# Performance work log

Measured on AMD Instinct MI355X. Metric: run time of the kernel, lower is better.

Reference implementation:

```python
import jax, jax.numpy as jnp
import numpy as np
import math

B, S, HID = 1, 4096, 2048
NH, NKV, HD = 16, 4, 128
SKETCH, TOPK = 640, 2048
EPS = 1e-6


def _dct_orthonormal(rows, cols, rng, sink=4, fsink=8):
    i = np.arange(rows)[:, None]
    j = np.arange(cols)[None, :]
    dct = np.cos(np.pi / cols * (j + 0.5) * i)
    dct[0, :] *= math.sqrt(1.0 / cols)
    dct[1:, :] *= math.sqrt(2.0 / cols)
    signs = rng.integers(0, 2, (1, cols)).astype(np.float64) * 2.0 - 1.0
    m = dct * signs
    m[:, :sink] *= 2.0
    m[:fsink, :] *= 1.5
    return m.astype(np.float32)


def setup_inputs() -> dict:
    key = jax.random.key(0)
    ks = jax.random.split(key, 8)
    rng = np.random.default_rng(0)
    # RoPE tables (b, s, 1, head_dim)
    pos = np.arange(S, dtype=np.float32)
    inv = 1.0 / (10000.0 ** (np.arange(0, HD, 2, dtype=np.float32) / HD))
    ang = pos[:, None] * inv[None, :]              # (S, HD/2)
    emb = np.concatenate([ang, ang], axis=-1)       # (S, HD)
    cos = np.broadcast_to(np.cos(emb)[None, :, None, :], (B, S, 1, HD)).copy()
    sin = np.broadcast_to(np.sin(emb)[None, :, None, :], (B, S, 1, HD)).copy()
    w = 0.02
    return {
        'hidden_states': jax.random.normal(ks[0], (B, S, HID), jnp.float32),
        'wq': jax.random.normal(ks[1], (HID, NH * HD), jnp.float32) * w,
        'wk': jax.random.normal(ks[2], (HID, NKV * HD), jnp.float32) * w,
        'wv': jax.random.normal(ks[3], (HID, NKV * HD), jnp.float32) * w,
        'wo': jax.random.normal(ks[4], (NH * HD, HID), jnp.float32) * w,
        'qn_w': jnp.ones((HD,), jnp.float32),
        'kn_w': jnp.ones((HD,), jnp.float32),
        's_w1': jax.random.normal(ks[5], (HID, 64), jnp.float32) * w,
        's_b1': jnp.zeros((64,), jnp.float32),
        's_w2': jax.random.normal(ks[6], (64, 1), jnp.float32) * w,
        's_b2': jnp.zeros((1,), jnp.float32),
        'sketch_scale': jnp.full((1,), 0.1, jnp.float32),
        'kron_a': jnp.asarray(_dct_orthonormal(20, 128, rng)),
        'kron_b': jnp.asarray(_dct_orthonormal(32, 256, rng)),
        'cos': jnp.asarray(cos),
        'sin': jnp.asarray(sin),
    }


def _rms_norm(x, w):
    var = jnp.mean(jnp.square(x), axis=-1, keepdims=True)
    return x * jax.lax.rsqrt(var + EPS) * w


def _rope(x, cos, sin):
    # x: (b, s, h, d); cos/sin: (b, s, 1, d)
    d2 = x.shape[-1] // 2
    rot = jnp.concatenate([-x[..., d2:], x[..., :d2]], axis=-1)
    return x * cos + rot * sin


def reference(hidden_states, wq, wk, wv, wo, qn_w, kn_w, s_w1, s_b1, s_w2, s_b2,
              sketch_scale, kron_a, kron_b, cos, sin):
    b, s, _ = hidden_states.shape
    # importance scorer with compression pressure bias
    logits = jnp.tanh(hidden_states @ s_w1 + s_b1) @ s_w2 + s_b2   # (b, s, 1)
    if s > SKETCH:
        logits = logits - math.log(s / SKETCH)
    iw = jax.nn.sigmoid(logits)                                    # (b, s, 1)

    q = (hidden_states @ wq).reshape(b, s, NH, HD)
    k = (hidden_states @ wk).reshape(b, s, NKV, HD)
    v = (hidden_states @ wv).reshape(b, s, NKV, HD)
    q = _rms_norm(q, qn_w)
    k = _rms_norm(k, kn_w)

    tk = min(s, TOPK)
    _, idx = jax.lax.top_k(logits[..., 0], tk)                     # (b, tk)
    ix = idx[:, :, None, None]
    k_detail = jnp.take_along_axis(k, ix, axis=1)                  # (b, tk, nkv, d)
    v_detail = jnp.take_along_axis(v, ix, axis=1)
    cos_det = jnp.take_along_axis(cos, ix, axis=1)                 # (b, tk, 1, d)
    sin_det = jnp.take_along_axis(sin, ix, axis=1)

    # Kronecker sketch of importance-weighted K/V over all tokens
    P = jnp.kron(kron_a, kron_b)[:, :s]                            # (640, s)
    kw = k * iw[..., None]
    vw = v * iw[..., None]
    k_sketch = jnp.einsum('bshd,ms->bmhd', kw, P) * sketch_scale
    v_sketch = jnp.einsum('bshd,ms->bmhd', vw, P) * sketch_scale

    q_rope = _rope(q, cos, sin)
    k_detail = _rope(k_detail, cos_det, sin_det)

    k_final = jnp.concatenate([k_detail, k_sketch], axis=1)        # (b, tk+640, nkv, d)
    v_final = jnp.concatenate([v_detail, v_sketch], axis=1)
    rep = NH // NKV
    k_final = jnp.repeat(k_final, rep, axis=2)                     # (b, L, nh, d)
    v_final = jnp.repeat(v_final, rep, axis=2)

    scores = jnp.einsum('bqhd,bkhd->bhqk', q_rope, k_final) / math.sqrt(HD)
    attn = jax.nn.softmax(scores, axis=-1)
    out = jnp.einsum('bhqk,bkhd->bqhd', attn, v_final).reshape(b, s, NH * HD)
    return out @ wo
```

## Files before the change

### kernel.cpp

```cpp
#include <hip/hip_runtime.h>
#include <math.h>

typedef _Float16 f16;
typedef f16 f16x8 __attribute__((ext_vector_type(8)));
typedef float f32x4 __attribute__((ext_vector_type(4)));

#define MFMA16(a,b,c) __builtin_amdgcn_mfma_f32_16x16x32_f16(a,b,c,0,0,0)

static __device__ __forceinline__ f16x8 ld8(const f16* p) { return *(const f16x8*)p; }

static __device__ __forceinline__ float exp2a(float x) {
    float r; asm("v_exp_f32 %0, %1" : "=v"(r) : "v"(x)); return r;
}

static __device__ __forceinline__ int xcd_remap(int flat, int nwg) {
    int q = nwg >> 3, r = nwg & 7;
    int xcd = flat & 7, pos = flat >> 3;
    return (xcd < r ? xcd * (q + 1) : r * (q + 1) + (xcd - r) * q) + pos;
}

#if __has_builtin(__builtin_amdgcn_global_load_lds)
#define GLL16(g, lptr) __builtin_amdgcn_global_load_lds((const __attribute__((address_space(1))) void*)(g), (__attribute__((address_space(3))) void*)(lptr), 16, 0, 0)
#else
#define GLL16(g, lptr) do { *(int4*)(lptr) = *(const int4*)(g); } while (0)
#endif

__global__ __launch_bounds__(256) void k_mlp1t(const float* __restrict__ h, const float* __restrict__ w1,
                                               const float* __restrict__ wq, const float* __restrict__ wk,
                                               const float* __restrict__ wv, const float* __restrict__ wo,
                                               double* __restrict__ part, f16* __restrict__ h16,
                                               f16* __restrict__ wqkvt, f16* __restrict__ wot) {
    int blk = blockIdx.x;
    int tid = threadIdx.x;
    if (blk < 512) {
        __shared__ float hs[64 * 68];
        __shared__ float ws[64 * 64];
        int rb = blk & 63, ks = blk >> 6;
        int jq = tid & 15, rt = tid >> 4;
        double acc[4][4];
        #pragma unroll
        for (int r = 0; r < 4; ++r)
            #pragma unroll
            for (int q = 0; q < 4; ++q) acc[r][q] = 0.0;

        float4 hreg[4], wreg[4];
        int hrow[4], hcq[4], wc[4], wq4[4];
        #pragma unroll
        for (int i = 0; i < 4; ++i) {
            int fl = i * 256 + tid;
            hrow[i] = fl >> 4; hcq[i] = fl & 15;
            wc[i] = fl >> 4;   wq4[i] = fl & 15;
        }
        #define LOADCH(c8) do {                                                                  \
            _Pragma("unroll")                                                                     \
            for (int i = 0; i < 4; ++i) {                                                         \
                hreg[i] = *(const float4*)&h[(size_t)(rb*64 + hrow[i])*2048 + ks*256 + (c8)*64 + hcq[i]*4]; \
                wreg[i] = *(const float4*)&w1[(size_t)(ks*256 + (c8)*64 + wc[i])*64 + wq4[i]*4];  \
            }                                                                                     \
        } while (0)

        LOADCH(0);
        for (int c8 = 0; c8 < 4; ++c8) {
            __syncthreads();
            #pragma unroll
            for (int i = 0; i < 4; ++i) {
                *(float4*)&hs[hrow[i]*68 + hcq[i]*4] = hreg[i];
                *(float4*)&ws[wc[i]*64 + wq4[i]*4] = wreg[i];
                const float* hp = (const float*)&hreg[i];
                f16 h4[4];
                #pragma unroll
                for (int z = 0; z < 4; ++z) h4[z] = (f16)hp[z];
                *(float*)&h16[(size_t)(rb*64 + hrow[i])*2048 + ks*256 + c8*64 + hcq[i]*4] = *(float*)h4;
                *(float*)(&h16[(size_t)(rb*64 + hrow[i])*2048 + ks*256 + c8*64 + hcq[i]*4 + 2]) = *(((float*)h4)+1);
            }
            __syncthreads();
            if (c8 < 3) LOADCH(c8 + 1);
            #pragma unroll 4
            for (int cg = 0; cg < 64; cg += 4) {
                float4 ha[4], wa[4];
                #pragma unroll
                for (int r = 0; r < 4; ++r) ha[r] = *(const float4*)&hs[(rt + 16*r)*68 + cg];
                #pragma unroll
                for (int cc = 0; cc < 4; ++cc) wa[cc] = *(const float4*)&ws[(cg + cc)*64 + jq*4];
                #pragma unroll
                for (int cc = 0; cc < 4; ++cc) {
                    const float* wap = (const float*)&wa[cc];
                    double wd0 = (double)wap[0], wd1 = (double)wap[1], wd2 = (double)wap[2], wd3 = (double)wap[3];
                    #pragma unroll
                    for (int r = 0; r < 4; ++r) {
                        double hv = (double)((const float*)&ha[r])[cc];
                        acc[r][0] = fma(hv, wd0, acc[r][0]);
                        acc[r][1] = fma(hv, wd1, acc[r][1]);
                        acc[r][2] = fma(hv, wd2, acc[r][2]);
                        acc[r][3] = fma(hv, wd3, acc[r][3]);
                    }
                }
            }
        }
        #pragma unroll
        for (int r = 0; r < 4; ++r)
            #pragma unroll
            for (int q = 0; q < 4; ++q)
                part[((size_t)ks*4096 + rb*64 + rt + 16*r)*64 + jq*4 + q] = acc[r][q];
        #undef LOADCH
    } else {
        __shared__ float tile[32][33];
        int tb = blk - 512;
        int bx = tb % 160;
        int y0 = (tb / 160) * 32;
        int tx = tid & 31, ty = tid >> 5;
        const float* in; int inCols, colBase, rowOff; f16* out;
        if (bx < 64)      { in = wq; inCols = 2048; colBase = bx * 32;        rowOff = colBase;        out = wqkvt; }
        else if (bx < 80) { in = wk; inCols = 512;  colBase = (bx - 64) * 32; rowOff = 2048 + colBase; out = wqkvt; }
        else if (bx < 96) { in = wv; inCols = 512;  colBase = (bx - 80) * 32; rowOff = 2560 + colBase; out = wqkvt; }
        else              { in = wo; inCols = 2048; colBase = (bx - 96) * 32; rowOff = colBase;        out = wot; }
        int x = colBase + tx;
        #pragma unroll
        for (int i = 0; i < 4; ++i)
            tile[ty + i*8][tx] = in[(size_t)(y0 + ty + i*8) * inCols + x];
        __syncthreads();
        #pragma unroll
        for (int i = 0; i < 4; ++i)
            out[(size_t)(rowOff + ty + i*8) * 2048 + y0 + tx] = (f16)tile[tx][ty + i*8];
    }
}

__global__ __launch_bounds__(256) void k_mlp2(const double* __restrict__ part, const float* __restrict__ b1,
                                              const float* __restrict__ w2, const float* __restrict__ b2,
                                              double* __restrict__ logitsD, float* __restrict__ iw) {
    int tid = threadIdx.x;
    int j = tid & 63, rq = tid >> 6;
    int row = blockIdx.x * 4 + rq;
    double s = 0.0;
    #pragma unroll
    for (int ks = 0; ks < 8; ++ks) s += part[((size_t)ks*4096 + row)*64 + j];
    double t = tanh(s + (double)b1[j]);
    double v = t * (double)w2[j];
    #pragma unroll
    for (int o = 32; o > 0; o >>= 1) v += __shfl_down(v, o);
    if (j == 0) {
        double lg = v + (double)b2[0] - 1.8562979903656263;
        logitsD[row] = lg;
        iw[row] = (float)(1.0 / (1.0 + exp(-lg)));
    }
}

__global__ __launch_bounds__(1024) void k_topk(const double* __restrict__ logitsD, int* __restrict__ sel) {
    __shared__ unsigned long long keys[4096];
    __shared__ unsigned int hist[2048];
    __shared__ unsigned int bcast[2];
    __shared__ unsigned int cA, cB;
    int tid = threadIdx.x;
    for (int i = tid; i < 4096; i += 1024) {
        unsigned long long u = (unsigned long long)__double_as_longlong(logitsD[i]);
        keys[i] = (u >> 63) ? ~u : (u | 0x8000000000000000ull);
    }
    if (tid == 0) { cA = 0; cB = 0; }
    unsigned long long Tpart = 0;
    unsigned int need = 2048;
    #pragma unroll 1
    for (int lvl = 0; lvl < 6; ++lvl) {
        int shift = (lvl < 5) ? (53 - 11*lvl) : 0;
        int width = (lvl < 5) ? 11 : 9;
        unsigned int nb = 1u << width;
        int hiShift = shift + width;
        for (int i = tid; i < (int)nb; i += 1024) hist[i] = 0;
        __syncthreads();
        for (int i = tid; i < 4096; i += 1024) {
            unsigned long long k = keys[i];
            bool cand = (lvl == 0) || ((k >> hiShift) == (Tpart >> hiShift));
            if (cand) atomicAdd(&hist[(unsigned int)(k >> shift) & (nb - 1u)], 1u);
        }
        __syncthreads();
        if (tid < 64) {
            int chunk = (int)nb >> 6;
            int base = (int)nb - (tid + 1) * chunk;
            unsigned int sum = 0;
            for (int jj = 0; jj < chunk; ++jj) sum += hist[base + jj];
            unsigned int pre = sum;
            #pragma unroll
            for (int o = 1; o < 64; o <<= 1) {
                unsigned int t = __shfl_up(pre, o);
                if (tid >= o) pre += t;
            }
            unsigned int preEx = pre - sum;
            if (preEx < need && need <= pre) {
                unsigned int cum = preEx;
                for (int jj = chunk - 1; jj >= 0; --jj) {
                    unsigned int c = hist[base + jj];
                    if (cum + c >= need) { bcast[0] = (unsigned int)(base + jj); bcast[1] = need - cum; break; }
                    cum += c;
                }
            }
        }
        __syncthreads();
        Tpart |= ((unsigned long long)bcast[0]) << shift;
        need = bcast[1];
        __syncthreads();
    }
    unsigned int G = 2048 - need;
    for (int i = tid; i < 4096; i += 1024) {
        unsigned long long k = keys[i];
        if (k > Tpart) { unsigned int p = atomicAdd(&cA, 1u); sel[p] = i; }
        else if (k == Tpart) { unsigned int q = atomicAdd(&cB, 1u); if (q < need) sel[G + q] = i; }
    }
}

__global__ __launch_bounds__(256) void k_gemm(const f16* __restrict__ A, const f16* __restrict__ Bt,
                                              float* __restrict__ C, int M, int N, int K) {
    __shared__ f16 As[128 * 32];
    __shared__ f16 Bs[128 * 32];
    int tid = threadIdx.x;
    int w = tid >> 6, l = tid & 63, lr = l & 15, lg = l >> 4;
    int wr = w >> 1, wc = w & 1;
    int nwg = gridDim.x * gridDim.y;
    int wid = xcd_remap(blockIdx.y * gridDim.x + blockIdx.x, nwg);
    int row0 = (wid / gridDim.x) * 128, col0 = (wid % gridDim.x) * 128;
    f32x4 zero = {0.f, 0.f, 0.f, 0.f};
    f32x4 acc[4][4];
    #pragma unroll
    for (int m = 0; m < 4; ++m)
        #pragma unroll
        for (int n = 0; n < 4; ++n) acc[m][n] = zero;
    for (int k0 = 0; k0 < K; k0 += 32) {
        #pragma unroll
        for (int p = 0; p < 2; ++p) {
            int id = p * 256 + tid;
            int r = id >> 2, c8 = (id & 3) * 8;
            GLL16(&A[(size_t)(row0 + r) * K + k0 + c8], &As[id * 8]);
            GLL16(&Bt[(size_t)(col0 + r) * K + k0 + c8], &Bs[id * 8]);
        }
        __syncthreads();
        f16x8 a[4], b[4];
        #pragma unroll
        for (int m = 0; m < 4; ++m) a[m] = ld8(&As[(wr*64 + m*16 + lr) * 32 + lg*8]);
        #pragma unroll
        for (int n = 0; n < 4; ++n) b[n] = ld8(&Bs[(wc*64 + n*16 + lr) * 32 + lg*8]);
        #pragma unroll
        for (int m = 0; m < 4; ++m)
            #pragma unroll
            for (int n = 0; n < 4; ++n)
                acc[m][n] = MFMA16(a[m], b[n], acc[m][n]);
        __syncthreads();
    }
    #pragma unroll
    for (int m = 0; m < 4; ++m)
        #pragma unroll
        for (int n = 0; n < 4; ++n)
            #pragma unroll
            for (int i = 0; i < 4; ++i)
                C[(size_t)(row0 + wr*64 + m*16 + lg*4 + i) * N + col0 + wc*64 + n*16 + lr] = acc[m][n][i];
}

__global__ __launch_bounds__(320) void k_norm(const float* __restrict__ qkv, const float* __restrict__ qnw,
                                              const float* __restrict__ knw, const float* __restrict__ cosb,
                                              const float* __restrict__ sinb, f16* __restrict__ qr,
                                              float* __restrict__ kn) {
    int s = blockIdx.x;
    int tid = threadIdx.x;
    if (tid < 256) {
        int h = tid >> 4, ln = tid & 15, d0 = ln * 8;
        const float* src = &qkv[(size_t)s * 3072 + h * 128 + d0];
        float4 a = *(const float4*)src, b = *(const float4*)(src + 4);
        float x[8] = {a.x,a.y,a.z,a.w,b.x,b.y,b.z,b.w};
        float ss = 0;
        #pragma unroll
        for (int j = 0; j < 8; ++j) ss += x[j]*x[j];
        ss += __shfl_xor(ss,1); ss += __shfl_xor(ss,2); ss += __shfl_xor(ss,4); ss += __shfl_xor(ss,8);
        float rn = rsqrtf(ss * (1.0f/128.0f) + 1e-6f);
        float xn[8];
        #pragma unroll
        for (int j = 0; j < 8; ++j) xn[j] = x[j] * rn * qnw[d0 + j];
        const float scl = 0.088388347648318447f * 1.4426950408889634f;
        f16x8 o;
        #pragma unroll
        for (int j = 0; j < 8; ++j) {
            float pr = __shfl_xor(xn[j], 8);
            float rot = (ln < 8) ? -pr : pr;
            int d = d0 + j;
            o[j] = (f16)((xn[j]*cosb[s*128 + d] + rot*sinb[s*128 + d]) * scl);
        }
        *(f16x8*)&qr[(size_t)s * 2048 + h * 128 + d0] = o;
    } else {
        int t2 = tid - 256;
        int h = t2 >> 4, ln = t2 & 15, d0 = ln * 8;
        const float* src = &qkv[(size_t)s * 3072 + 2048 + h * 128 + d0];
        float4 a = *(const float4*)src, b = *(const float4*)(src + 4);
        float x[8] = {a.x,a.y,a.z,a.w,b.x,b.y,b.z,b.w};
        float ss = 0;
        #pragma unroll
        for (int j = 0; j < 8; ++j) ss += x[j]*x[j];
        ss += __shfl_xor(ss,1); ss += __shfl_xor(ss,2); ss += __shfl_xor(ss,4); ss += __shfl_xor(ss,8);
        float rn = rsqrtf(ss * (1.0f/128.0f) + 1e-6f);
        float o[8];
        #pragma unroll
        for (int j = 0; j < 8; ++j) o[j] = x[j] * rn * knw[d0 + j];
        float* dst = &kn[(size_t)s*512 + h*128 + d0];
        *(float4*)dst = make_float4(o[0],o[1],o[2],o[3]);
        *(float4*)(dst+4) = make_float4(o[4],o[5],o[6],o[7]);
    }
}

__global__ __launch_bounds__(256) void k_gather_sketch(const int* __restrict__ sel, const float* __restrict__ kn,
                                                       const float* __restrict__ qkv, const float* __restrict__ cosb,
                                                       const float* __restrict__ sinb, const float* __restrict__ iw,
                                                       const float* __restrict__ kronb, f16* __restrict__ Kf,
                                                       f16* __restrict__ VfT, float* __restrict__ T) {
    int bid = blockIdx.x;
    if (bid < 1024) {
        int which = bid >> 9, inner = bid & 511;
        int mb = inner & 31, sa = inner >> 5;
        int c0 = threadIdx.x * 2;
        float a0 = 0, a1 = 0;
        for (int sb = 0; sb < 256; ++sb) {
            int s = sa * 256 + sb;
            float wgt = kronb[mb * 256 + sb] * iw[s];
            const float* src = which ? &qkv[(size_t)s*3072 + 2560] : &kn[(size_t)s*512];
            a0 += wgt * src[c0];
            a1 += wgt * src[c0 + 1];
        }
        float* dst = &T[(size_t)((which*32 + mb)*16 + sa) * 512 + c0];
        dst[0] = a0; dst[1] = a1;
    } else {
        int j = (bid - 1024) * 2 + (threadIdx.x >> 7);
        int t = threadIdx.x & 127;
        int s = sel[j];
        float c = cosb[s*128 + t], sn = sinb[s*128 + t];
        #pragma unroll
        for (int h = 0; h < 4; ++h) {
            float x  = kn[(size_t)s*512 + h*128 + t];
            float pr = kn[(size_t)s*512 + h*128 + (t ^ 64)];
            float rot = (t < 64) ? -pr : pr;
            Kf[(size_t)(h*2688 + j) * 128 + t] = (f16)(x*c + rot*sn);
            float v = qkv[(size_t)s*3072 + 2560 + h*128 + t];
            VfT[(size_t)h*128*2688 + (size_t)t*2688 + j] = (f16)v;
        }
    }
}

__global__ __launch_bounds__(256) void k_sketch2(const float* __restrict__ T, const float* __restrict__ krona,
                                                 const float* __restrict__ sscale, f16* __restrict__ Kf,
                                                 f16* __restrict__ VfT) {
    int m = blockIdx.x;
    int which = blockIdx.y;
    int ma = m >> 5, mb = m & 31;
    int c0 = threadIdx.x * 2;
    float sc = sscale[0];
    float a0 = 0, a1 = 0;
    #pragma unroll
    for (int sa = 0; sa < 16; ++sa) {
        float ka = krona[ma * 128 + sa];
        const float* t = &T[(size_t)((which*32 + mb)*16 + sa) * 512 + c0];
        a0 += ka * t[0];
        a1 += ka * t[1];
    }
    a0 *= sc; a1 *= sc;
    int key = 2048 + m;
    int h0 = c0 >> 7, d = c0 & 127;
    if (which == 0) {
        Kf[(size_t)(h0*2688 + key)*128 + d]     = (f16)a0;
        Kf[(size_t)(h0*2688 + key)*128 + d + 1] = (f16)a1;
    } else {
        VfT[(size_t)h0*128*2688 + (size_t)d*2688 + key]       = (f16)a0;
        VfT[(size_t)h0*128*2688 + (size_t)(d+1)*2688 + key]   = (f16)a1;
    }
}

__global__ __launch_bounds__(256, 2) void k_attn(const f16* __restrict__ qr, const f16* __restrict__ Kf,
                                                 const f16* __restrict__ VfT, f16* __restrict__ out16) {
    __shared__ f16 KT[2][64 * 128];
    __shared__ f16 VT[2][128 * 64];
    __shared__ f16 P[4][32 * 64];
    int nwg = gridDim.x * gridDim.y;
    int wid = xcd_remap(blockIdx.y * gridDim.x + blockIdx.x, nwg);
    int qt = wid % gridDim.x, h = wid / gridDim.x;
    int kvh = h >> 2;
    int tid = threadIdx.x;
    int w = tid >> 6, l = tid & 63, lr = l & 15, lg = l >> 4;
    int q0 = qt * 128 + w * 32;
    const char* Kb = (const char*)(Kf + (size_t)kvh * 2688 * 128);
    const char* Vb = (const char*)(VfT + (size_t)kvh * 128 * 2688);
    char* Pw = (char*)&P[w][0];

    int koff[4], voff[2];
    #pragma unroll
    for (int c = 0; c < 4; ++c) koff[c] = (c*64 + lg*16) ^ ((lr & 7) << 5);
    #pragma unroll
    for (int kw = 0; kw < 2; ++kw) voff[kw] = (kw*64 + lg*16) ^ ((lr & 7) << 4);
    int psw = (lr & 7) << 4;

    int L0 = tid * 16;

    f16x8 aq[2][4];
    #pragma unroll
    for (int hh = 0; hh < 2; ++hh)
        #pragma unroll
        for (int c = 0; c < 4; ++c)
            aq[hh][c] = ld8(&qr[(size_t)(q0 + hh*16 + lr) * 2048 + h*128 + c*32 + lg*8]);

    f32x4 zero = {0.f,0.f,0.f,0.f};
    f32x4 o0[8], o1[8];
    #pragma unroll
    for (int f = 0; f < 8; ++f) { o0[f] = zero; o1[f] = zero; }
    float m0[4], m1[4], ls0[4], ls1[4];
    #pragma unroll
    for (int i = 0; i < 4; ++i) { m0[i] = -1e30f; m1[i] = -1e30f; ls0[i] = 0.f; ls1[i] = 0.f; }

    #define STAGE(buf, kt)  do {                                                          \
        _Pragma("unroll")                                                                  \
        for (int i_ = 0; i_ < 4; ++i_) {                                                   \
            int L = L0 + i_*4096;                                                          \
            int krow = L >> 8, kbc = L & 255;                                              \
            GLL16(Kb + (size_t)((kt) + krow)*256 + (kbc ^ ((krow & 7) << 5)),              \
                  (char*)&KT[buf][0] + L);                                                 \
            int vd = L >> 7, vbc = L & 127;                                                \
            GLL16(Vb + (size_t)vd*5376 + (size_t)(kt)*2 + (vbc ^ ((vd & 7) << 4)),         \
                  (char*)&VT[buf][0] + L);                                                 \
        }                                                                                  \
    } while (0)

    STAGE(0, 0);
    asm volatile("s_waitcnt vmcnt(0)" ::: "memory");
    __syncthreads();

    for (int t = 0; t < 42; ++t) {
        int cur = t & 1;
        if (t < 41) STAGE(cur ^ 1, (t + 1) * 64);
        const char* Kc = (const char*)&KT[cur][0];
        const char* Vc = (const char*)&VT[cur][0];

        f32x4 s0[4], s1[4];
        #pragma unroll
        for (int tt = 0; tt < 4; ++tt) { s0[tt] = zero; s1[tt] = zero; }
        __builtin_amdgcn_s_setprio(1);
        #pragma unroll
        for (int tt = 0; tt < 4; ++tt) {
            #pragma unroll
            for (int c = 0; c < 4; ++c) {
                f16x8 kb = ld8((const f16*)(Kc + (tt*16 + lr)*256 + koff[c]));
                s0[tt] = MFMA16(aq[0][c], kb, s0[tt]);
                s1[tt] = MFMA16(aq[1][c], kb, s1[tt]);
            }
        }
        __builtin_amdgcn_s_setprio(0);

        float tl0[4], tl1[4];
        bool need = false;
        #pragma unroll
        for (int i = 0; i < 4; ++i) {
            tl0[i] = fmaxf(fmaxf(s0[0][i], s0[1][i]), fmaxf(s0[2][i], s0[3][i]));
            tl1[i] = fmaxf(fmaxf(s1[0][i], s1[1][i]), fmaxf(s1[2][i], s1[3][i]));
            need = need || (tl0[i] > m0[i]+8.f) || (tl1[i] > m1[i]+8.f);
        }
        if (__any(need)) {
            f32x4 cf0, cf1;
            #pragma unroll
            for (int i = 0; i < 4; ++i) {
                float a = tl0[i];
                a = fmaxf(a, __shfl_xor(a, 1)); a = fmaxf(a, __shfl_xor(a, 2));
                a = fmaxf(a, __shfl_xor(a, 4)); a = fmaxf(a, __shfl_xor(a, 8));
                float mn0 = fmaxf(m0[i], a);
                cf0[i] = exp2a(m0[i] - mn0); m0[i] = mn0; ls0[i] *= cf0[i];
                float b = tl1[i];
                b = fmaxf(b, __shfl_xor(b, 1)); b = fmaxf(b, __shfl_xor(b, 2));
                b = fmaxf(b, __shfl_xor(b, 4)); b = fmaxf(b, __shfl_xor(b, 8));
                float mn1 = fmaxf(m1[i], b);
                cf1[i] = exp2a(m1[i] - mn1); m1[i] = mn1; ls1[i] *= cf1[i];
            }
            #pragma unroll
            for (int f = 0; f < 8; ++f) { o0[f] *= cf0; o1[f] *= cf1; }
        }
        #pragma unroll
        for (int tt = 0; tt < 4; ++tt)
            #pragma unroll
            for (int i = 0; i < 4; ++i) {
                int r0 = lg*4 + i;
                float p0 = exp2a(s0[tt][i] - m0[i]);
                ls0[i] += p0;
                *(f16*)(Pw + ((r0*128 + (tt*16+lr)*2) ^ ((r0 & 7) << 4))) = (f16)p0;
                int r1 = 16 + r0;
                float p1 = exp2a(s1[tt][i] - m1[i]);
                ls1[i] += p1;
                *(f16*)(Pw + ((r1*128 + (tt*16+lr)*2) ^ ((r1 & 7) << 4))) = (f16)p1;
            }
        asm volatile("s_waitcnt lgkmcnt(0)" ::: "memory");
        __builtin_amdgcn_sched_barrier(0);

        __builtin_amdgcn_s_setprio(1);
        #pragma unroll
        for (int kw = 0; kw < 2; ++kw) {
            f16x8 pa0 = *(const f16x8*)(Pw + ((lr*128 + kw*64 + lg*16) ^ psw));
            f16x8 pa1 = *(const f16x8*)(Pw + (((16+lr)*128 + kw*64 + lg*16) ^ psw));
            #pragma unroll
            for (int f = 0; f < 8; ++f) {
                f16x8 vb = ld8((const f16*)(Vc + (f*16 + lr)*128 + voff[kw]));
                o0[f] = MFMA16(pa0, vb, o0[f]);
                o1[f] = MFMA16(pa1, vb, o1[f]);
            }
        }
        __builtin_amdgcn_s_setprio(0);
        asm volatile("s_waitcnt vmcnt(0)" ::: "memory");
        __syncthreads();
    }

    #pragma unroll
    for (int i = 0; i < 4; ++i) {
        float a = ls0[i];
        a += __shfl_xor(a, 1); a += __shfl_xor(a, 2); a += __shfl_xor(a, 4); a += __shfl_xor(a, 8);
        float inv0 = 1.0f / a;
        float b = ls1[i];
        b += __shfl_xor(b, 1); b += __shfl_xor(b, 2); b += __shfl_xor(b, 4); b += __shfl_xor(b, 8);
        float inv1 = 1.0f / b;
        #pragma unroll
        for (int f = 0; f < 8; ++f) {
            out16[(size_t)(q0 + lg*4 + i) * 2048 + h*128 + f*16 + lr]      = (f16)(o0[f][i] * inv0);
            out16[(size_t)(q0 + 16 + lg*4 + i) * 2048 + h*128 + f*16 + lr] = (f16)(o1[f][i] * inv1);
        }
    }
    #undef STAGE
}

extern "C" void kernel_launch(void* const* d_in, const int* in_sizes, int n_in,
                              void* d_out, int out_size, void* d_ws, size_t ws_size,
                              hipStream_t stream) {
    const float* h     = (const float*)d_in[0];
    const float* wq    = (const float*)d_in[1];
    const float* wk    = (const float*)d_in[2];
    const float* wv    = (const float*)d_in[3];
    const float* wo    = (const float*)d_in[4];
    const float* qnw   = (const float*)d_in[5];
    const float* knw   = (const float*)d_in[6];
    const float* sw1   = (const float*)d_in[7];
    const float* sb1   = (const float*)d_in[8];
    const float* sw2   = (const float*)d_in[9];
    const float* sb2   = (const float*)d_in[10];
    const float* sscal = (const float*)d_in[11];
    const float* ka    = (const float*)d_in[12];
    const float* kb    = (const float*)d_in[13];
    const float* cosb  = (const float*)d_in[14];
    const float* sinb  = (const float*)d_in[15];
    float* outp = (float*)d_out;

    char* ws = (char*)d_ws;
    size_t off = 0;
    f16*    h16    = (f16*)(ws + off);   off += (size_t)4096*2048*2;
    f16*    wqkvt  = (f16*)(ws + off);   off += (size_t)3072*2048*2;
    f16*    wot    = (f16*)(ws + off);   off += (size_t)2048*2048*2;
    float*  qkvraw = (float*)(ws + off); off += (size_t)4096*3072*4;
    f16*    qr     = (f16*)(ws + off);   off += (size_t)4096*2048*2;
    float*  kn     = (float*)(ws + off); off += (size_t)4096*512*4;
    f16*    attn16 = (f16*)(ws + off);   off += (size_t)4096*2048*2;
    float*  T      = (float*)(ws + off); off += (size_t)2*32*16*512*4;
    f16*    Kf     = (f16*)(ws + off);   off += (size_t)4*2688*128*2;
    f16*    VfT    = (f16*)(ws + off);   off += (size_t)4*128*2688*2;
    double* logitsD= (double*)(ws + off);off += (size_t)4096*8;
    float*  iw     = (float*)(ws + off); off += (size_t)4096*4;
    int*    sel    = (int*)(ws + off);   off += (size_t)2048*4;
    double* part   = (double*)qkvraw;

    k_mlp1t<<<10752, 256, 0, stream>>>(h, sw1, wq, wk, wv, wo, part, h16, wqkvt, wot);
    k_mlp2<<<1024, 256, 0, stream>>>(part, sb1, sw2, sb2, logitsD, iw);
    k_topk<<<1, 1024, 0, stream>>>(logitsD, sel);
    k_gemm<<<dim3(24,32), 256, 0, stream>>>(h16, wqkvt, qkvraw, 4096, 3072, 2048);
    k_norm<<<4096, 320, 0, stream>>>(qkvraw, qnw, knw, cosb, sinb, qr, kn);
    k_gather_sketch<<<2048, 256, 0, stream>>>(sel, kn, qkvraw, cosb, sinb, iw, kb, Kf, VfT, T);
    k_sketch2<<<dim3(640,2), 256, 0, stream>>>(T, ka, sscal, Kf, VfT);
    k_attn<<<dim3(32,16), 256, 0, stream>>>(qr, Kf, VfT, attn16);
    k_gemm<<<dim3(16,32), 256, 0, stream>>>(attn16, wot, outp, 4096, 2048, 2048);
}
```

Baseline: 397.3 us.

## Fuse RMSNorm and RoPE into QKV projection GEMM epilogue

Fuses the per-head Q/K RMSNorm and Q RoPE into the QKV GEMM epilogue. Each 128-column tile is one head, so sum of squares is reduced across lanes and waves through shared memory, and the RoPE partner element is read back from an LDS buffer. This removes the separate normalization kernel and the fp32 round trip of Q/K through global memory. Only V is still written raw. The cost is extra LDS use (32KB xbuf), which may lower GEMM occupancy, and uncoalesced scattered epilogue stores.

Result: slower. 452.8 us (+14.0%).

```diff
diff --git a/kernel.cpp b/kernel.cpp
--- a/kernel.cpp
+++ b/kernel.cpp
@@ -206,6 +206,121 @@
     }
 }
 
+__global__ __launch_bounds__(256) void k_gemm_qkv(const f16* __restrict__ A, const f16* __restrict__ Bt,
+                                                  float* __restrict__ qkvV, const float* __restrict__ qnw,
+                                                  const float* __restrict__ knw, const float* __restrict__ cosb,
+                                                  const float* __restrict__ sinb, f16* __restrict__ qr,
+                                                  float* __restrict__ kn) {
+    __shared__ f16 As[128 * 32];
+    __shared__ f16 Bs[128 * 32];
+    __shared__ float ssb[256];
+    __shared__ f16 xbuf[128 * 128];
+    const int K = 2048;
+    int tid = threadIdx.x;
+    int w = tid >> 6, l = tid & 63, lr = l & 15, lg = l >> 4;
+    int wr = w >> 1, wc = w & 1;
+    int nwg = gridDim.x * gridDim.y;
+    int wid = xcd_remap(blockIdx.y * gridDim.x + blockIdx.x, nwg);
+    int row0 = (wid / gridDim.x) * 128, col0 = (wid % gridDim.x) * 128;
+    f32x4 zero = {0.f, 0.f, 0.f, 0.f};
+    f32x4 acc[4][4];
+    #pragma unroll
+    for (int m = 0; m < 4; ++m)
+        #pragma unroll
+        for (int n = 0; n < 4; ++n) acc[m][n] = zero;
+    for (int k0 = 0; k0 < K; k0 += 32) {
+        #pragma unroll
+        for (int p = 0; p < 2; ++p) {
+            int id = p * 256 + tid;
+            int r = id >> 2, c8 = (id & 3) * 8;
+            GLL16(&A[(size_t)(row0 + r) * K + k0 + c8], &As[id * 8]);
+            GLL16(&Bt[(size_t)(col0 + r) * K + k0 + c8], &Bs[id * 8]);
+        }
+        __syncthreads();
+        f16x8 a[4], b[4];
+        #pragma unroll
+        for (int m = 0; m < 4; ++m) a[m] = ld8(&As[(wr*64 + m*16 + lr) * 32 + lg*8]);
+        #pragma unroll
+        for (int n = 0; n < 4; ++n) b[n] = ld8(&Bs[(wc*64 + n*16 + lr) * 32 + lg*8]);
+        #pragma unroll
+        for (int m = 0; m < 4; ++m)
+            #pragma unroll
+            for (int n = 0; n < 4; ++n)
+                acc[m][n] = MFMA16(a[m], b[n], acc[m][n]);
+        __syncthreads();
+    }
+
+    if (col0 >= 2560) {
+        #pragma unroll
+        for (int m = 0; m < 4; ++m)
+            #pragma unroll
+            for (int n = 0; n < 4; ++n)
+                #pragma unroll
+                for (int i = 0; i < 4; ++i)
+                    qkvV[(size_t)(row0 + wr*64 + m*16 + lg*4 + i) * 3072 + col0 + wc*64 + n*16 + lr] = acc[m][n][i];
+        return;
+    }
+    float ss[4][4];
+    #pragma unroll
+    for (int m = 0; m < 4; ++m)
+        #pragma unroll
+        for (int i = 0; i < 4; ++i) {
+            float s = 0;
+            #pragma unroll
+            for (int n = 0; n < 4; ++n) s += acc[m][n][i] * acc[m][n][i];
+            s += __shfl_xor(s, 1); s += __shfl_xor(s, 2);
+            s += __shfl_xor(s, 4); s += __shfl_xor(s, 8);
+            ss[m][i] = s;
+        }
+    if (lr == 0) {
+        #pragma unroll
+        for (int m = 0; m < 4; ++m)
+            #pragma unroll
+            for (int i = 0; i < 4; ++i)
+                ssb[wc*128 + wr*64 + m*16 + lg*4 + i] = ss[m][i];
+    }
+    __syncthreads();
+    bool isK = (col0 >= 2048);
+    #pragma unroll
+    for (int m = 0; m < 4; ++m)
+        #pragma unroll
+        for (int i = 0; i < 4; ++i) {
+            int ridx = wr*64 + m*16 + lg*4 + i;
+            float rn = rsqrtf((ssb[ridx] + ssb[128 + ridx]) * (1.0f/128.0f) + 1e-6f);
+            int r = row0 + ridx;
+            #pragma unroll
+            for (int n = 0; n < 4; ++n) {
+                int dd = wc*64 + n*16 + lr;
+                if (isK) {
+                    kn[(size_t)r*512 + (col0 - 2048) + dd] = acc[m][n][i] * rn * knw[dd];
+                } else {
+                    float xn = acc[m][n][i] * rn * qnw[dd];
+                    acc[m][n][i] = xn;
+                    xbuf[ridx*128 + dd] = (f16)xn;
+                }
+            }
+        }
+    if (!isK) {
+        __syncthreads();
+        const float scl = 0.088388347648318447f * 1.4426950408889634f;
+        #pragma unroll
+        for (int m = 0; m < 4; ++m)
+            #pragma unroll
+            for (int i = 0; i < 4; ++i) {
+                int ridx = wr*64 + m*16 + lg*4 + i;
+                int r = row0 + ridx;
+                #pragma unroll
+                for (int n = 0; n < 4; ++n) {
+                    int dd = wc*64 + n*16 + lr;
+                    float p = (float)xbuf[ridx*128 + (dd ^ 64)];
+                    float rot = (dd < 64) ? -p : p;
+                    qr[(size_t)r*2048 + col0 + dd] =
+                        (f16)((acc[m][n][i]*cosb[r*128 + dd] + rot*sinb[r*128 + dd]) * scl);
+                }
+            }
+    }
+}
+
 __global__ __launch_bounds__(256) void k_gemm(const f16* __restrict__ A, const f16* __restrict__ Bt,
                                               float* __restrict__ C, int M, int N, int K) {
     __shared__ f16 As[128 * 32];
@@ -250,55 +365,6 @@
             #pragma unroll
             for (int i = 0; i < 4; ++i)
                 C[(size_t)(row0 + wr*64 + m*16 + lg*4 + i) * N + col0 + wc*64 + n*16 + lr] = acc[m][n][i];
-}
-
-__global__ __launch_bounds__(320) void k_norm(const float* __restrict__ qkv, const float* __restrict__ qnw,
-                                              const float* __restrict__ knw, const float* __restrict__ cosb,
-                                              const float* __restrict__ sinb, f16* __restrict__ qr,
-                                              float* __restrict__ kn) {
-    int s = blockIdx.x;
-    int tid = threadIdx.x;
-    if (tid < 256) {
-        int h = tid >> 4, ln = tid & 15, d0 = ln * 8;
-        const float* src = &qkv[(size_t)s * 3072 + h * 128 + d0];
-        float4 a = *(const float4*)src, b = *(const float4*)(src + 4);
-        float x[8] = {a.x,a.y,a.z,a.w,b.x,b.y,b.z,b.w};
-        float ss = 0;
-        #pragma unroll
-        for (int j = 0; j < 8; ++j) ss += x[j]*x[j];
-        ss += __shfl_xor(ss,1); ss += __shfl_xor(ss,2); ss += __shfl_xor(ss,4); ss += __shfl_xor(ss,8);
-        float rn = rsqrtf(ss * (1.0f/128.0f) + 1e-6f);
-        float xn[8];
-        #pragma unroll
-        for (int j = 0; j < 8; ++j) xn[j] = x[j] * rn * qnw[d0 + j];
-        const float scl = 0.088388347648318447f * 1.4426950408889634f;
-        f16x8 o;
-        #pragma unroll
-        for (int j = 0; j < 8; ++j) {
-            float pr = __shfl_xor(xn[j], 8);
-            float rot = (ln < 8) ? -pr : pr;
-            int d = d0 + j;
-            o[j] = (f16)((xn[j]*cosb[s*128 + d] + rot*sinb[s*128 + d]) * scl);
-        }
-        *(f16x8*)&qr[(size_t)s * 2048 + h * 128 + d0] = o;
-    } else {
-        int t2 = tid - 256;
-        int h = t2 >> 4, ln = t2 & 15, d0 = ln * 8;
-        const float* src = &qkv[(size_t)s * 3072 + 2048 + h * 128 + d0];
-        float4 a = *(const float4*)src, b = *(const float4*)(src + 4);
-        float x[8] = {a.x,a.y,a.z,a.w,b.x,b.y,b.z,b.w};
-        float ss = 0;
-        #pragma unroll
-        for (int j = 0; j < 8; ++j) ss += x[j]*x[j];
-        ss += __shfl_xor(ss,1); ss += __shfl_xor(ss,2); ss += __shfl_xor(ss,4); ss += __shfl_xor(ss,8);
-        float rn = rsqrtf(ss * (1.0f/128.0f) + 1e-6f);
-        float o[8];
-        #pragma unroll
-        for (int j = 0; j < 8; ++j) o[j] = x[j] * rn * knw[d0 + j];
-        float* dst = &kn[(size_t)s*512 + h*128 + d0];
-        *(float4*)dst = make_float4(o[0],o[1],o[2],o[3]);
-        *(float4*)(dst+4) = make_float4(o[4],o[5],o[6],o[7]);
-    }
 }
 
 __global__ __launch_bounds__(256) void k_gather_sketch(const int* __restrict__ sel, const float* __restrict__ kn,
@@ -561,8 +627,7 @@
     k_mlp1t<<<10752, 256, 0, stream>>>(h, sw1, wq, wk, wv, wo, part, h16, wqkvt, wot);
     k_mlp2<<<1024, 256, 0, stream>>>(part, sb1, sw2, sb2, logitsD, iw);
     k_topk<<<1, 1024, 0, stream>>>(logitsD, sel);
-    k_gemm<<<dim3(24,32), 256, 0, stream>>>(h16, wqkvt, qkvraw, 4096, 3072, 2048);
-    k_norm<<<4096, 320, 0, stream>>>(qkvraw, qnw, knw, cosb, sinb, qr, kn);
+    k_gemm_qkv<<<dim3(24,32), 256, 0, stream>>>(h16, wqkvt, qkvraw, qnw, knw, cosb, sinb, qr, kn);
     k_gather_sketch<<<2048, 256, 0, stream>>>(sel, kn, qkvraw, cosb, sinb, iw, kb, Kf, VfT, T);
     k_sketch2<<<dim3(640,2), 256, 0, stream>>>(T, ka, sscal, Kf, VfT);
     k_attn<<<dim3(32,16), 256, 0, stream>>>(qr, Kf, VfT, attn16);
```
